# Kernel optimization log

Hardware: AMD Instinct MI355X
Metric: run time of the kernel (lower is better)

## Reference

```python
import jax, jax.numpy as jnp
import numpy as np

D = 2048      # hidden_size
S = 2048      # seq_len (batch packed, batch=1)
H = 16        # num_attention_heads
QL = 1536     # q_lora_rank
KVL = 512     # kv_lora_rank (latent dim, also v head size)
DN = 128      # qk_nope_head_dim
DR = 64       # qk_rope_head_dim
DV = 128      # v_head_dim
I = 8192      # mlp intermediate
EPS = 1e-6
SCALE = (DN + DR) ** -0.5  # softmax_scale = q_head_dim**-0.5 (no yarn mscale)


def rmsnorm(x, w):
    return x * jax.lax.rsqrt(jnp.mean(x * x, axis=-1, keepdims=True) + EPS) * w


def rotate_half(x):
    h = x.shape[-1] // 2
    return jnp.concatenate([-x[..., h:], x[..., :h]], axis=-1)


def setup_inputs() -> dict:
    key = jax.random.key(0)
    ks = jax.random.split(key, 10)
    s = 0.02
    # real RoPE tables (rotate_half layout)
    inv_freq = 1.0 / (10000.0 ** (jnp.arange(0, DR, 2, dtype=jnp.float32) / DR))
    t = jnp.arange(S, dtype=jnp.float32)
    emb = jnp.concatenate([jnp.outer(t, inv_freq)] * 2, axis=-1)  # [S, DR]
    return {
        'hidden_states': jax.random.normal(ks[0], (1, S, D), dtype=jnp.float32),
        'cos': jnp.cos(emb),
        'sin': jnp.sin(emb),
        'ln1_w': jnp.ones((D,), jnp.float32),
        'q_a_w': jax.random.normal(ks[1], (D, QL)) * s,
        'q_a_ln_w': jnp.ones((QL,), jnp.float32),
        'q_b_w': jax.random.normal(ks[2], (QL, H * (DN + DR))) * s,
        'kv_a_w': jax.random.normal(ks[3], (D, KVL + DR)) * s,
        'kv_a_ln_w': jnp.ones((KVL,), jnp.float32),
        'kc_w': jax.random.normal(ks[4], (H, DN, KVL)) * s,
        'vc_w': jax.random.normal(ks[5], (H, KVL, DV)) * s,
        'o_w': jax.random.normal(ks[6], (H * DV, D)) * s,
        'ln2_w': jnp.ones((D,), jnp.float32),
        'gate_up_w': jax.random.normal(ks[7], (D, 2 * I)) * s,
        'down_w': jax.random.normal(ks[8], (I, D)) * s,
    }


def reference(hidden_states, cos, sin, ln1_w, q_a_w, q_a_ln_w, q_b_w,
              kv_a_w, kv_a_ln_w, kc_w, vc_w, o_w, ln2_w, gate_up_w, down_w):
    residual = hidden_states
    h = rmsnorm(hidden_states, ln1_w)[0]                      # [S, D]
    # --- Q path: low-rank down + RMSNorm + up, split nope/rope ---
    q = rmsnorm(h @ q_a_w, q_a_ln_w) @ q_b_w                  # [S, H*(DN+DR)]
    q = q.reshape(S, H, DN + DR)
    q_nope, q_pe = q[..., :DN], q[..., DN:]
    # kc BMM: absorb W_UK, project q_nope into latent dim     # [S, H, KVL]
    q_lat = jnp.einsum('shd,hdc->shc', q_nope, kc_w)
    # --- KV path: compressed latent + shared rope key ---
    kv = h @ kv_a_w                                           # [S, KVL+DR]
    k_lat = rmsnorm(kv[:, :KVL], kv_a_ln_w)                   # [S, KVL] (also V)
    k_pe = kv[:, KVL:]                                        # [S, DR]
    # --- RoPE on the rope split only ---
    q_pe = q_pe * cos[:, None, :] + rotate_half(q_pe) * sin[:, None, :]
    k_pe = k_pe * cos + rotate_half(k_pe) * sin
    # --- latent MQA attention: q/k dim = KVL+DR, v dim = KVL ---
    qf = jnp.concatenate([q_lat, q_pe], axis=-1)              # [S, H, KVL+DR]
    kf = jnp.concatenate([k_lat, k_pe], axis=-1)              # [S, KVL+DR]
    scores = jnp.einsum('shc,tc->hst', qf, kf) * SCALE        # [H, S, S]
    causal = jnp.tril(jnp.ones((S, S), dtype=bool))
    scores = jnp.where(causal, scores, jnp.float32(-1e30))
    attn = jax.nn.softmax(scores, axis=-1)
    o_lat = jnp.einsum('hst,tc->shc', attn, k_lat)            # [S, H, KVL]
    # vc BMM: latent -> v_head_dim
    o = jnp.einsum('shc,hcv->shv', o_lat, vc_w).reshape(S, H * DV)
    attn_out = (o @ o_w)[None]                                # [1, S, D]
    hidden = residual + attn_out
    # --- dense SwiGLU MLP ---
    x2 = rmsnorm(hidden, ln2_w)
    gu = x2 @ gate_up_w
    mlp = (jax.nn.silu(gu[..., :I]) * gu[..., I:]) @ down_w
    return hidden + mlp
```

## Files before the change

### kernel.cpp

```cpp
#include <hip/hip_runtime.h>
#include <stdint.h>


#define S_   2048
#define D_   2048
#define H_   16
#define QL_  1536
#define KVL_ 512
#define DN_  128
#define DR_  64
#define DV_  128
#define I_   8192
#define SCALE_ 0.07216878364870323f

typedef __bf16 bf16x8 __attribute__((ext_vector_type(8)));
typedef float f32x4 __attribute__((ext_vector_type(4)));

__device__ __forceinline__ unsigned short f2bf(float f) {
  unsigned int u = __builtin_bit_cast(unsigned int, f);
  u += 0x7fffu + ((u >> 16) & 1u);
  return (unsigned short)(u >> 16);
}
__device__ __forceinline__ float bf2f(unsigned short b) {
  unsigned int u = ((unsigned int)b) << 16;
  return __builtin_bit_cast(float, u);
}

__device__ __forceinline__ float block_sum256(float v) {
  __shared__ float red[4];
  #pragma unroll
  for (int o = 32; o; o >>= 1) v += __shfl_xor(v, o);
  __syncthreads();
  if ((threadIdx.x & 63) == 0) red[threadIdx.x >> 6] = v;
  __syncthreads();
  return red[0] + red[1] + red[2] + red[3];
}
__device__ __forceinline__ float block_max256(float v) {
  __shared__ float red[4];
  #pragma unroll
  for (int o = 32; o; o >>= 1) v = fmaxf(v, __shfl_xor(v, o));
  __syncthreads();
  if ((threadIdx.x & 63) == 0) red[threadIdx.x >> 6] = v;
  __syncthreads();
  return fmaxf(fmaxf(red[0], red[1]), fmaxf(red[2], red[3]));
}

__device__ __forceinline__ void gload_lds16(const void* g, void* l) {
  void* gn = const_cast<void*>(g);
  __builtin_amdgcn_global_load_lds(
      (__attribute__((address_space(1))) void*)gn,
      (__attribute__((address_space(3))) void*)l, 16, 0, 0);
}

template <int OUT_BF16, int ADD_RES, int TRI, int CK>
__global__ __launch_bounds__(256) void gemm_bt(
    const unsigned short* __restrict__ A, const unsigned short* __restrict__ Bt,
    void* __restrict__ C, const float* __restrict__ R, float scale,
    int M, int N, int K, int lda, int ldb, int ldc,
    long sA, long sB, long sC) {
  __shared__ unsigned short As[128 * 32];
  __shared__ unsigned short Bs[128 * 32];
  const int b = blockIdx.z;
  const unsigned short* Ab = A + (long)b * sA;
  const unsigned short* Bb = Bt + (long)b * sB;
  int bx = blockIdx.x, by = blockIdx.y;
  if (TRI) {
    const int t = blockIdx.x;
    int i = (int)((sqrtf(8.f * t + 1.f) - 1.f) * 0.5f);
    while ((i + 1) * (i + 2) / 2 <= t) ++i;
    while (i * (i + 1) / 2 > t) --i;
    by = i;
    bx = t - i * (i + 1) / 2;
  }
  const int m0 = by * 128, n0 = bx * 128;
  if (CK) K = min(K, m0 + 128);
  const int tid = threadIdx.x, w = tid >> 6, lane = tid & 63;
  const int wm = (w >> 1) * 64, wn = (w & 1) * 64;
  const int fr = lane & 15;
  const int fq = lane >> 4;

  f32x4 acc[4][4] = {};

  for (int k0 = 0; k0 < K; k0 += 32) {
    #pragma unroll
    for (int i = 0; i < 2; ++i) {
      const int c = w * 128 + i * 64 + lane;
      const int row = c >> 2, q = c & 3;
      gload_lds16(Ab + (long)(m0 + row) * lda + k0 + q * 8,
                  As + (w * 128 + i * 64) * 8);
      gload_lds16(Bb + (long)(n0 + row) * ldb + k0 + q * 8,
                  Bs + (w * 128 + i * 64) * 8);
    }
    __syncthreads();
    bf16x8 af[4], bfr[4];
    #pragma unroll
    for (int i = 0; i < 4; ++i)
      af[i] = *(const bf16x8*)(As + (wm + i * 16 + fr) * 32 + fq * 8);
    #pragma unroll
    for (int j = 0; j < 4; ++j)
      bfr[j] = *(const bf16x8*)(Bs + (wn + j * 16 + fr) * 32 + fq * 8);
    #pragma unroll
    for (int i = 0; i < 4; ++i)
      #pragma unroll
      for (int j = 0; j < 4; ++j)
        acc[i][j] = __builtin_amdgcn_mfma_f32_16x16x32_bf16(af[i], bfr[j],
                                                            acc[i][j], 0, 0, 0);
    __syncthreads();
  }

  const long cb = (long)b * sC;
  #pragma unroll
  for (int i = 0; i < 4; ++i) {
    const int row0 = m0 + wm + i * 16 + fq * 4;
    #pragma unroll
    for (int j = 0; j < 4; ++j) {
      const int col = n0 + wn + j * 16 + fr;
      if (col < N) {
        #pragma unroll
        for (int r = 0; r < 4; ++r) {
          const long idx = cb + (long)(row0 + r) * ldc + col;
          float v = acc[i][j][r] * scale;
          if (ADD_RES) v += R[idx];
          if (OUT_BF16) ((unsigned short*)C)[idx] = f2bf(v);
          else          ((float*)C)[idx] = v;
        }
      }
    }
  }
}

__global__ void transpose_f2b(const float* __restrict__ in,
                              unsigned short* __restrict__ out, int Rr, int Cc,
                              long sIn, long sOut) {
  const int b = blockIdx.z;
  in += (long)b * sIn;
  out += (long)b * sOut;
  __shared__ float t[32][33];
  const int c0 = blockIdx.x * 32, r0 = blockIdx.y * 32;
  const int tx = threadIdx.x, ty = threadIdx.y;
  #pragma unroll
  for (int i = 0; i < 4; ++i)
    t[ty + i * 8][tx] = in[(long)(r0 + ty + i * 8) * Cc + c0 + tx];
  __syncthreads();
  #pragma unroll
  for (int i = 0; i < 4; ++i)
    out[(long)(c0 + ty + i * 8) * Rr + r0 + tx] = f2bf(t[tx][ty + i * 8]);
}

__global__ void rmsnorm_k(const float* __restrict__ x, const float* __restrict__ w,
                          unsigned short* __restrict__ y, int C) {
  const int row = blockIdx.x, tid = threadIdx.x;
  const float* xr = x + (long)row * C;
  float ss = 0.f;
  for (int c = tid; c < C; c += 256) { float v = xr[c]; ss += v * v; }
  ss = block_sum256(ss);
  const float rms = rsqrtf(ss / C + 1e-6f);
  for (int c = tid; c < C; c += 256)
    y[(long)row * C + c] = f2bf(xr[c] * rms * w[c]);
}

__global__ void q_post(const float* __restrict__ q, const float* __restrict__ cs,
                       const float* __restrict__ sn, unsigned short* __restrict__ qnope,
                       unsigned short* __restrict__ qf) {
  const int s = blockIdx.x, tid = threadIdx.x;
  const float* qr = q + (long)s * 3072;
  for (int c = tid; c < 3072; c += 256) {
    const int h = c / 192, d = c % 192;
    if (d < 128) {
      qnope[(long)s * 2048 + h * 128 + d] = f2bf(qr[c]);
    } else {
      const int j = d - 128;
      const float x = qr[c];
      const float rot = (j < 32) ? -qr[h * 192 + 128 + j + 32]
                                 :  qr[h * 192 + 128 + j - 32];
      const float v = x * cs[s * 64 + j] + rot * sn[s * 64 + j];
      qf[(long)h * (S_ * 576) + (long)s * 576 + 512 + j] = f2bf(v);
    }
  }
}

__global__ void kv_post(const float* __restrict__ kv, const float* __restrict__ w,
                        const float* __restrict__ cs, const float* __restrict__ sn,
                        unsigned short* __restrict__ kf, unsigned short* __restrict__ klt) {
  const int s = blockIdx.x, tid = threadIdx.x;
  const float* kr = kv + (long)s * 576;
  float ss = 0.f;
  for (int c = tid; c < 512; c += 256) { float v = kr[c]; ss += v * v; }
  ss = block_sum256(ss);
  const float rms = rsqrtf(ss / 512.f + 1e-6f);
  for (int c = tid; c < 576; c += 256) {
    if (c < 512) {
      const float v = kr[c] * rms * w[c];
      const unsigned short bv = f2bf(v);
      kf[(long)s * 576 + c] = bv;
      klt[(long)c * S_ + s] = bv;
    } else {
      const int j = c - 512;
      const float x = kr[c];
      const float rot = (j < 32) ? -kr[512 + j + 32] : kr[512 + j - 32];
      kf[(long)s * 576 + c] = f2bf(x * cs[s * 64 + j] + rot * sn[s * 64 + j]);
    }
  }
}

__global__ void softmax_causal_ip(unsigned short* __restrict__ sc, long hstride) {
  const int row = blockIdx.x, tid = threadIdx.x;
  unsigned short* sr = sc + (long)blockIdx.z * hstride + (long)row * S_;
  const int n = row + 1;
  const int kmax = ((row >> 7) + 1) << 7;
  float mx = -1e30f;
  for (int c = tid; c < n; c += 256) mx = fmaxf(mx, bf2f(sr[c]));
  mx = block_max256(mx);
  float e[8];
  float sum = 0.f;
  #pragma unroll
  for (int k = 0; k < 8; ++k) {
    const int c = tid + k * 256;
    if (c < n) { e[k] = __expf(bf2f(sr[c]) - mx); sum += e[k]; }
  }
  sum = block_sum256(sum);
  const float inv = 1.f / sum;
  #pragma unroll
  for (int k = 0; k < 8; ++k) {
    const int c = tid + k * 256;
    if (c < n) sr[c] = f2bf(e[k] * inv);
    else if (c < kmax) sr[c] = 0;
  }
}

__global__ void add_rms(const float* __restrict__ resid, const float* __restrict__ attn,
                        const float* __restrict__ w, float* __restrict__ hidden,
                        unsigned short* __restrict__ x2) {
  const int s = blockIdx.x, tid = threadIdx.x;
  float ss = 0.f;
  for (int c = tid; c < D_; c += 256) {
    const float v = resid[(long)s * D_ + c] + attn[(long)s * D_ + c];
    hidden[(long)s * D_ + c] = v;
    ss += v * v;
  }
  ss = block_sum256(ss);
  const float rms = rsqrtf(ss / D_ + 1e-6f);
  for (int c = tid; c < D_; c += 256) {
    const float v = resid[(long)s * D_ + c] + attn[(long)s * D_ + c];
    x2[(long)s * D_ + c] = f2bf(v * rms * w[c]);
  }
}

__global__ void silu_mul(const unsigned short* __restrict__ gu,
                         unsigned short* __restrict__ out) {
  const long total = (long)S_ * I_ / 8;
  for (long t = (long)blockIdx.x * 256 + threadIdx.x; t < total;
       t += (long)gridDim.x * 256) {
    const long s = t >> 10, c8 = (t & 1023) * 8;
    const uint4 gv = *(const uint4*)(gu + s * (2 * I_) + c8);
    const uint4 uv = *(const uint4*)(gu + s * (2 * I_) + I_ + c8);
    const unsigned int* gp = (const unsigned int*)&gv;
    const unsigned int* up = (const unsigned int*)&uv;
    uint4 ov;
    unsigned int* op = (unsigned int*)&ov;
    #pragma unroll
    for (int k = 0; k < 4; ++k) {
      const float g0 = bf2f((unsigned short)(gp[k] & 0xffff));
      const float g1 = bf2f((unsigned short)(gp[k] >> 16));
      const float u0 = bf2f((unsigned short)(up[k] & 0xffff));
      const float u1 = bf2f((unsigned short)(up[k] >> 16));
      const float r0 = g0 / (1.f + __expf(-g0)) * u0;
      const float r1 = g1 / (1.f + __expf(-g1)) * u1;
      op[k] = (unsigned int)f2bf(r0) | ((unsigned int)f2bf(r1) << 16);
    }
    *(uint4*)(out + t * 8) = ov;
  }
}

extern "C" void kernel_launch(void* const* d_in, const int* in_sizes, int n_in,
                              void* d_out, int out_size, void* d_ws, size_t ws_size,
                              hipStream_t stream) {
  const float* hs   = (const float*)d_in[0];
  const float* cs   = (const float*)d_in[1];
  const float* sn   = (const float*)d_in[2];
  const float* ln1  = (const float*)d_in[3];
  const float* qaw  = (const float*)d_in[4];
  const float* qaln = (const float*)d_in[5];
  const float* qbw  = (const float*)d_in[6];
  const float* kvaw = (const float*)d_in[7];
  const float* kvln = (const float*)d_in[8];
  const float* kcw  = (const float*)d_in[9];
  const float* vcw  = (const float*)d_in[10];
  const float* ow   = (const float*)d_in[11];
  const float* ln2  = (const float*)d_in[12];
  const float* guw  = (const float*)d_in[13];
  const float* dww  = (const float*)d_in[14];
  float* out = (float*)d_out;
  char* ws = (char*)d_ws;

  unsigned short* hbf   = (unsigned short*)(ws + 0);
  float*          qa    = (float*)(ws + 8388608);
  unsigned short* qan   = (unsigned short*)(ws + 20971520);
  float*          q     = (float*)(ws + 27262976);
  unsigned short* qnope = (unsigned short*)(ws + 52428800);
  unsigned short* qf    = (unsigned short*)(ws + 60817408);
  float*          kv    = (float*)(ws + 98566144);
  unsigned short* kf    = (unsigned short*)(ws + 103284736);
  unsigned short* klt   = (unsigned short*)(ws + 105644032);
  unsigned short* wt2   = (unsigned short*)(ws + 123731968);
  unsigned short* wt    = (unsigned short*)(ws + 125829120);
  unsigned short* sc    = (unsigned short*)(ws + 0);
  unsigned short* olat  = (unsigned short*)(ws + 125829120);
  unsigned short* obf   = (unsigned short*)(ws + 0);
  float*          attn  = (float*)(ws + 8388608);
  float*          hidden= (float*)(ws + 33554432);
  unsigned short* x2    = (unsigned short*)(ws + 50331648);
  unsigned short* gu    = (unsigned short*)(ws + 58720256);
  unsigned short* mlp   = (unsigned short*)(ws + 0);
  unsigned short* wtB   = (unsigned short*)(ws + 125829120);

  const dim3 B256(256), Bt32(32, 8);

  rmsnorm_k<<<S_, B256, 0, stream>>>(hs, ln1, hbf, D_);
  transpose_f2b<<<dim3(QL_/32, D_/32, 1), Bt32, 0, stream>>>(qaw, wt, D_, QL_, 0, 0);
  gemm_bt<0,0,0,0><<<dim3(QL_/128, S_/128, 1), B256, 0, stream>>>(
      hbf, wt, qa, nullptr, 1.f, S_, QL_, D_, D_, D_, QL_, 0, 0, 0);
  rmsnorm_k<<<S_, B256, 0, stream>>>(qa, qaln, qan, QL_);
  transpose_f2b<<<dim3(3072/32, QL_/32, 1), Bt32, 0, stream>>>(qbw, wt, QL_, 3072, 0, 0);
  gemm_bt<0,0,0,0><<<dim3(3072/128, S_/128, 1), B256, 0, stream>>>(
      qan, wt, q, nullptr, 1.f, S_, 3072, QL_, QL_, QL_, 3072, 0, 0, 0);
  q_post<<<S_, B256, 0, stream>>>(q, cs, sn, qnope, qf);
  transpose_f2b<<<dim3(576/32, D_/32, 1), Bt32, 0, stream>>>(kvaw, wt, D_, 576, 0, 0);
  gemm_bt<0,0,0,0><<<dim3(5, S_/128, 1), B256, 0, stream>>>(
      hbf, wt, kv, nullptr, 1.f, S_, 576, D_, D_, D_, 576, 0, 0, 0);
  kv_post<<<S_, B256, 0, stream>>>(kv, kvln, cs, sn, kf, klt);
  transpose_f2b<<<dim3(512/32, 128/32, H_), Bt32, 0, stream>>>(kcw, wt, 128, 512, 65536, 65536);
  transpose_f2b<<<dim3(128/32, 512/32, H_), Bt32, 0, stream>>>(vcw, wt2, 512, 128, 65536, 65536);
  gemm_bt<1,0,0,0><<<dim3(4, S_/128, H_), B256, 0, stream>>>(
      qnope, wt, qf, nullptr, 1.f, S_, 512, 128, 2048, 128, 576,
      128, 65536, (long)S_ * 576);
  for (int g = 0; g < 4; ++g) {
    const unsigned short* qfg = qf + (long)g * 4 * S_ * 576;
    gemm_bt<1,0,1,0><<<dim3(136, 1, 4), B256, 0, stream>>>(
        qfg, kf, sc, nullptr, SCALE_, S_, S_, 576, 576, 576, S_,
        (long)S_ * 576, 0, (long)S_ * S_);
    softmax_causal_ip<<<dim3(S_, 1, 4), B256, 0, stream>>>(sc, (long)S_ * S_);
    gemm_bt<1,0,0,1><<<dim3(4, 16, 4), B256, 0, stream>>>(
        sc, klt, olat + (long)g * 4 * S_ * 512, nullptr, 1.f,
        S_, 512, S_, S_, S_, 512, (long)S_ * S_, 0, (long)S_ * 512);
  }
  gemm_bt<1,0,0,0><<<dim3(1, S_/128, H_), B256, 0, stream>>>(
      olat, wt2, obf, nullptr, 1.f, S_, 128, 512, 512, 512, 2048,
      (long)S_ * 512, 65536, 128);
  transpose_f2b<<<dim3(D_/32, D_/32, 1), Bt32, 0, stream>>>(ow, wtB, D_, D_, 0, 0);
  gemm_bt<0,0,0,0><<<dim3(D_/128, S_/128, 1), B256, 0, stream>>>(
      obf, wtB, attn, nullptr, 1.f, S_, D_, D_, D_, D_, D_, 0, 0, 0);
  add_rms<<<S_, B256, 0, stream>>>(hs, attn, ln2, hidden, x2);
  transpose_f2b<<<dim3(2 * I_ / 32, D_/32, 1), Bt32, 0, stream>>>(guw, wtB, D_, 2 * I_, 0, 0);
  gemm_bt<1,0,0,0><<<dim3(2 * I_ / 128, S_/128, 1), B256, 0, stream>>>(
      x2, wtB, gu, nullptr, 1.f, S_, 2 * I_, D_, D_, D_, 2 * I_, 0, 0, 0);
  silu_mul<<<2048, B256, 0, stream>>>(gu, mlp);
  transpose_f2b<<<dim3(D_/32, I_/32, 1), Bt32, 0, stream>>>(dww, wtB, I_, D_, 0, 0);
  gemm_bt<0,1,0,0><<<dim3(D_/128, S_/128, 1), B256, 0, stream>>>(
      mlp, wtB, out, hidden, 1.f, S_, D_, I_, I_, I_, D_, 0, 0, 0);
}
```

Baseline: 1.323 ms.

## Widen GEMM K-tile with swizzled LDS, fuse SiLU-mul and residual into epilogues

The GEMM K step goes from 32 to 64, and the LDS layout is XOR-swizzled to avoid bank conflicts, which halves the barriers per K. The gate/up weight is transposed into interleaved order so the GEMM epilogue computes silu(gate)*up with a lane shuffle and writes the MLP input directly. The o_proj residual add is fused into the GEMM epilogue, followed by a plain rmsnorm, which removes add_rms. Attention runs in 2 groups of 8 heads instead of 4 groups of 4, and the workspace is re-laid out to fit. The wider tile doubles LDS use, which may reduce occupancy.

```diff
diff --git a/kernel.cpp b/kernel.cpp
--- a/kernel.cpp
+++ b/kernel.cpp
@@ -52,17 +52,15 @@
       (__attribute__((address_space(3))) void*)l, 16, 0, 0);
 }
 
-template <int OUT_BF16, int ADD_RES, int TRI, int CK>
+template <int OUT, int ADD_RES, int TRI, int CK>
 __global__ __launch_bounds__(256) void gemm_bt(
     const unsigned short* __restrict__ A, const unsigned short* __restrict__ Bt,
     void* __restrict__ C, const float* __restrict__ R, float scale,
     int M, int N, int K, int lda, int ldb, int ldc,
     long sA, long sB, long sC) {
-  __shared__ unsigned short As[128 * 32];
-  __shared__ unsigned short Bs[128 * 32];
+  __shared__ unsigned short As[128 * 64];
+  __shared__ unsigned short Bs[128 * 64];
   const int b = blockIdx.z;
-  const unsigned short* Ab = A + (long)b * sA;
-  const unsigned short* Bb = Bt + (long)b * sB;
   int bx = blockIdx.x, by = blockIdx.y;
   if (TRI) {
     const int t = blockIdx.x;
@@ -78,33 +76,46 @@
   const int wm = (w >> 1) * 64, wn = (w & 1) * 64;
   const int fr = lane & 15;
   const int fq = lane >> 4;
+  const int sr = lane >> 3;
+  const int sch = (lane & 7) ^ sr;
+  const unsigned short* Ab = A + (long)b * sA;
+  const unsigned short* Bb = Bt + (long)b * sB;
+  long aOff[4], bOff[4];
+  #pragma unroll
+  for (int i = 0; i < 4; ++i) {
+    const int row = w * 32 + i * 8 + sr;
+    aOff[i] = (long)(m0 + row) * lda + sch * 8;
+    bOff[i] = (long)(n0 + row) * ldb + sch * 8;
+  }
+  const int ca0 = fq ^ (fr & 7);
+  const int ca1 = (4 + fq) ^ (fr & 7);
 
   f32x4 acc[4][4] = {};
 
-  for (int k0 = 0; k0 < K; k0 += 32) {
+  for (int k0 = 0; k0 < K; k0 += 64) {
     #pragma unroll
-    for (int i = 0; i < 2; ++i) {
-      const int c = w * 128 + i * 64 + lane;
-      const int row = c >> 2, q = c & 3;
-      gload_lds16(Ab + (long)(m0 + row) * lda + k0 + q * 8,
-                  As + (w * 128 + i * 64) * 8);
-      gload_lds16(Bb + (long)(n0 + row) * ldb + k0 + q * 8,
-                  Bs + (w * 128 + i * 64) * 8);
+    for (int i = 0; i < 4; ++i) {
+      gload_lds16(Ab + aOff[i] + k0, As + (w * 32 + i * 8) * 64);
+      gload_lds16(Bb + bOff[i] + k0, Bs + (w * 32 + i * 8) * 64);
     }
     __syncthreads();
-    bf16x8 af[4], bfr[4];
     #pragma unroll
-    for (int i = 0; i < 4; ++i)
-      af[i] = *(const bf16x8*)(As + (wm + i * 16 + fr) * 32 + fq * 8);
-    #pragma unroll
-    for (int j = 0; j < 4; ++j)
-      bfr[j] = *(const bf16x8*)(Bs + (wn + j * 16 + fr) * 32 + fq * 8);
-    #pragma unroll
-    for (int i = 0; i < 4; ++i)
+    for (int s = 0; s < 2; ++s) {
+      const int cc = s ? ca1 : ca0;
+      bf16x8 af[4], bf[4];
+      #pragma unroll
+      for (int i = 0; i < 4; ++i)
+        af[i] = *(const bf16x8*)(As + (wm + i * 16 + fr) * 64 + cc * 8);
       #pragma unroll
       for (int j = 0; j < 4; ++j)
-        acc[i][j] = __builtin_amdgcn_mfma_f32_16x16x32_bf16(af[i], bfr[j],
-                                                            acc[i][j], 0, 0, 0);
+        bf[j] = *(const bf16x8*)(Bs + (wn + j * 16 + fr) * 64 + cc * 8);
+      #pragma unroll
+      for (int i = 0; i < 4; ++i)
+        #pragma unroll
+        for (int j = 0; j < 4; ++j)
+          acc[i][j] = __builtin_amdgcn_mfma_f32_16x16x32_bf16(af[i], bf[j],
+                                                              acc[i][j], 0, 0, 0);
+    }
     __syncthreads();
   }
 
@@ -115,14 +126,23 @@
     #pragma unroll
     for (int j = 0; j < 4; ++j) {
       const int col = n0 + wn + j * 16 + fr;
-      if (col < N) {
-        #pragma unroll
-        for (int r = 0; r < 4; ++r) {
-          const long idx = cb + (long)(row0 + r) * ldc + col;
-          float v = acc[i][j][r] * scale;
-          if (ADD_RES) v += R[idx];
-          if (OUT_BF16) ((unsigned short*)C)[idx] = f2bf(v);
-          else          ((float*)C)[idx] = v;
+      #pragma unroll
+      for (int r = 0; r < 4; ++r) {
+        float v = acc[i][j][r] * scale;
+        if (OUT == 2) {
+          const float o = __shfl_xor(v, 1);
+          const float res = v / (1.f + __expf(-v)) * o;
+          if (((fr & 1) == 0) && col < N)
+            ((unsigned short*)C)[cb + (long)(row0 + r) * ldc + (col >> 1)] =
+                f2bf(res);
+        } else {
+          if (col < N) {
+            const long idx = cb + (long)(row0 + r) * ldc + col;
+            float vv = v;
+            if (ADD_RES) vv += R[idx];
+            if (OUT == 1) ((unsigned short*)C)[idx] = f2bf(vv);
+            else          ((float*)C)[idx] = vv;
+          }
         }
       }
     }
@@ -145,6 +165,23 @@
   #pragma unroll
   for (int i = 0; i < 4; ++i)
     out[(long)(c0 + ty + i * 8) * Rr + r0 + tx] = f2bf(t[tx][ty + i * 8]);
+}
+
+__global__ void transpose_f2b_ilv(const float* __restrict__ in,
+                                  unsigned short* __restrict__ out) {
+  __shared__ float t[32][33];
+  const int c0 = blockIdx.x * 32, r0 = blockIdx.y * 32;
+  const int tx = threadIdx.x, ty = threadIdx.y;
+  #pragma unroll
+  for (int i = 0; i < 4; ++i)
+    t[ty + i * 8][tx] = in[(long)(r0 + ty + i * 8) * (2 * I_) + c0 + tx];
+  __syncthreads();
+  #pragma unroll
+  for (int i = 0; i < 4; ++i) {
+    const int c = c0 + ty + i * 8;
+    const int n = ((c & (I_ - 1)) << 1) | (c >> 13);
+    out[(long)n * D_ + r0 + tx] = f2bf(t[tx][ty + i * 8]);
+  }
 }
 
 __global__ void rmsnorm_k(const float* __restrict__ x, const float* __restrict__ w,
@@ -228,50 +265,6 @@
   }
 }
 
-__global__ void add_rms(const float* __restrict__ resid, const float* __restrict__ attn,
-                        const float* __restrict__ w, float* __restrict__ hidden,
-                        unsigned short* __restrict__ x2) {
-  const int s = blockIdx.x, tid = threadIdx.x;
-  float ss = 0.f;
-  for (int c = tid; c < D_; c += 256) {
-    const float v = resid[(long)s * D_ + c] + attn[(long)s * D_ + c];
-    hidden[(long)s * D_ + c] = v;
-    ss += v * v;
-  }
-  ss = block_sum256(ss);
-  const float rms = rsqrtf(ss / D_ + 1e-6f);
-  for (int c = tid; c < D_; c += 256) {
-    const float v = resid[(long)s * D_ + c] + attn[(long)s * D_ + c];
-    x2[(long)s * D_ + c] = f2bf(v * rms * w[c]);
-  }
-}
-
-__global__ void silu_mul(const unsigned short* __restrict__ gu,
-                         unsigned short* __restrict__ out) {
-  const long total = (long)S_ * I_ / 8;
-  for (long t = (long)blockIdx.x * 256 + threadIdx.x; t < total;
-       t += (long)gridDim.x * 256) {
-    const long s = t >> 10, c8 = (t & 1023) * 8;
-    const uint4 gv = *(const uint4*)(gu + s * (2 * I_) + c8);
-    const uint4 uv = *(const uint4*)(gu + s * (2 * I_) + I_ + c8);
-    const unsigned int* gp = (const unsigned int*)&gv;
-    const unsigned int* up = (const unsigned int*)&uv;
-    uint4 ov;
-    unsigned int* op = (unsigned int*)&ov;
-    #pragma unroll
-    for (int k = 0; k < 4; ++k) {
-      const float g0 = bf2f((unsigned short)(gp[k] & 0xffff));
-      const float g1 = bf2f((unsigned short)(gp[k] >> 16));
-      const float u0 = bf2f((unsigned short)(up[k] & 0xffff));
-      const float u1 = bf2f((unsigned short)(up[k] >> 16));
-      const float r0 = g0 / (1.f + __expf(-g0)) * u0;
-      const float r1 = g1 / (1.f + __expf(-g1)) * u1;
-      op[k] = (unsigned int)f2bf(r0) | ((unsigned int)f2bf(r1) << 16);
-    }
-    *(uint4*)(out + t * 8) = ov;
-  }
-}
-
 extern "C" void kernel_launch(void* const* d_in, const int* in_sizes, int n_in,
                               void* d_out, int out_size, void* d_ws, size_t ws_size,
                               hipStream_t stream) {
@@ -298,21 +291,18 @@
   unsigned short* qan   = (unsigned short*)(ws + 20971520);
   float*          q     = (float*)(ws + 27262976);
   unsigned short* qnope = (unsigned short*)(ws + 52428800);
-  unsigned short* qf    = (unsigned short*)(ws + 60817408);
-  float*          kv    = (float*)(ws + 98566144);
-  unsigned short* kf    = (unsigned short*)(ws + 103284736);
-  unsigned short* klt   = (unsigned short*)(ws + 105644032);
-  unsigned short* wt2   = (unsigned short*)(ws + 123731968);
-  unsigned short* wt    = (unsigned short*)(ws + 125829120);
   unsigned short* sc    = (unsigned short*)(ws + 0);
-  unsigned short* olat  = (unsigned short*)(ws + 125829120);
+  unsigned short* qf    = (unsigned short*)(ws + 67108864);
+  float*          kv    = (float*)(ws + 104857600);
+  unsigned short* kf    = (unsigned short*)(ws + 109576192);
+  unsigned short* klt   = (unsigned short*)(ws + 111935488);
+  unsigned short* wt2   = (unsigned short*)(ws + 114032640);
+  unsigned short* wt    = (unsigned short*)(ws + 116129792);
+  unsigned short* olat  = (unsigned short*)(ws + 116129792);
   unsigned short* obf   = (unsigned short*)(ws + 0);
-  float*          attn  = (float*)(ws + 8388608);
-  float*          hidden= (float*)(ws + 33554432);
-  unsigned short* x2    = (unsigned short*)(ws + 50331648);
-  unsigned short* gu    = (unsigned short*)(ws + 58720256);
-  unsigned short* mlp   = (unsigned short*)(ws + 0);
-  unsigned short* wtB   = (unsigned short*)(ws + 125829120);
+  float*          hidden= (float*)(ws + 8388608);
+  unsigned short* x2    = (unsigned short*)(ws + 25165824);
+  unsigned short* mlp   = (unsigned short*)(ws + 33554432);
 
   const dim3 B256(256), Bt32(32, 8);
 
@@ -334,28 +324,27 @@
   gemm_bt<1,0,0,0><<<dim3(4, S_/128, H_), B256, 0, stream>>>(
       qnope, wt, qf, nullptr, 1.f, S_, 512, 128, 2048, 128, 576,
       128, 65536, (long)S_ * 576);
-  for (int g = 0; g < 4; ++g) {
-    const unsigned short* qfg = qf + (long)g * 4 * S_ * 576;
-    gemm_bt<1,0,1,0><<<dim3(136, 1, 4), B256, 0, stream>>>(
+  for (int g = 0; g < 2; ++g) {
+    const unsigned short* qfg = qf + (long)g * 8 * S_ * 576;
+    gemm_bt<1,0,1,0><<<dim3(136, 1, 8), B256, 0, stream>>>(
         qfg, kf, sc, nullptr, SCALE_, S_, S_, 576, 576, 576, S_,
         (long)S_ * 576, 0, (long)S_ * S_);
-    softmax_causal_ip<<<dim3(S_, 1, 4), B256, 0, stream>>>(sc, (long)S_ * S_);
-    gemm_bt<1,0,0,1><<<dim3(4, 16, 4), B256, 0, stream>>>(
-        sc, klt, olat + (long)g * 4 * S_ * 512, nullptr, 1.f,
+    softmax_causal_ip<<<dim3(S_, 1, 8), B256, 0, stream>>>(sc, (long)S_ * S_);
+    gemm_bt<1,0,0,1><<<dim3(4, 16, 8), B256, 0, stream>>>(
+        sc, klt, olat + (long)g * 8 * S_ * 512, nullptr, 1.f,
         S_, 512, S_, S_, S_, 512, (long)S_ * S_, 0, (long)S_ * 512);
   }
   gemm_bt<1,0,0,0><<<dim3(1, S_/128, H_), B256, 0, stream>>>(
       olat, wt2, obf, nullptr, 1.f, S_, 128, 512, 512, 512, 2048,
       (long)S_ * 512, 65536, 128);
-  transpose_f2b<<<dim3(D_/32, D_/32, 1), Bt32, 0, stream>>>(ow, wtB, D_, D_, 0, 0);
-  gemm_bt<0,0,0,0><<<dim3(D_/128, S_/128, 1), B256, 0, stream>>>(
-      obf, wtB, attn, nullptr, 1.f, S_, D_, D_, D_, D_, D_, 0, 0, 0);
-  add_rms<<<S_, B256, 0, stream>>>(hs, attn, ln2, hidden, x2);
-  transpose_f2b<<<dim3(2 * I_ / 32, D_/32, 1), Bt32, 0, stream>>>(guw, wtB, D_, 2 * I_, 0, 0);
-  gemm_bt<1,0,0,0><<<dim3(2 * I_ / 128, S_/128, 1), B256, 0, stream>>>(
-      x2, wtB, gu, nullptr, 1.f, S_, 2 * I_, D_, D_, D_, 2 * I_, 0, 0, 0);
-  silu_mul<<<2048, B256, 0, stream>>>(gu, mlp);
-  transpose_f2b<<<dim3(D_/32, I_/32, 1), Bt32, 0, stream>>>(dww, wtB, I_, D_, 0, 0);
+  transpose_f2b<<<dim3(D_/32, D_/32, 1), Bt32, 0, stream>>>(ow, wt, D_, D_, 0, 0);
   gemm_bt<0,1,0,0><<<dim3(D_/128, S_/128, 1), B256, 0, stream>>>(
-      mlp, wtB, out, hidden, 1.f, S_, D_, I_, I_, I_, D_, 0, 0, 0);
-}
+      obf, wt, hidden, hs, 1.f, S_, D_, D_, D_, D_, D_, 0, 0, 0);
+  rmsnorm_k<<<S_, B256, 0, stream>>>(hidden, ln2, x2, D_);
+  transpose_f2b_ilv<<<dim3(2 * I_ / 32, D_/32, 1), Bt32, 0, stream>>>(guw, wt);
+  gemm_bt<2,0,0,0><<<dim3(2 * I_ / 128, S_/128, 1), B256, 0, stream>>>(
+      x2, wt, mlp, nullptr, 1.f, S_, 2 * I_, D_, D_, D_, I_, 0, 0, 0);
+  transpose_f2b<<<dim3(D_/32, I_/32, 1), Bt32, 0, stream>>>(dww, wt, I_, D_, 0, 0);
+  gemm_bt<0,1,0,0><<<dim3(D_/128, S_/128, 1), B256, 0, stream>>>(
+      mlp, wt, out, hidden, 1.f, S_, D_, I_, I_, I_, D_, 0, 0, 0);
+}
```

Result: faster. 1.081 ms (-18.3%).
